# Optimization experiments

Hardware: AMD Instinct MI355X
Metric: run time of the kernel (lower is better)

Reference implementation:

```python
import jax, jax.numpy as jnp
import numpy as np

N_NODES = 50000

def setup_inputs() -> dict:
    key = jax.random.key(0)
    ks = jax.random.split(key, 4)
    x = jax.random.normal(ks[0], (N_NODES, 64), dtype=jnp.float32)
    edge_index = jax.random.randint(ks[1], (2, 800000), 0, N_NODES, dtype=jnp.int64)
    W1 = jax.random.normal(ks[2], (64, 128), dtype=jnp.float32) * (1.0 / np.sqrt(64))
    b1 = jnp.zeros((128,), dtype=jnp.float32)
    W2 = jax.random.normal(ks[3], (128, 64), dtype=jnp.float32) * (1.0 / np.sqrt(128))
    b2 = jnp.zeros((64,), dtype=jnp.float32)
    eps = jnp.zeros((1,), dtype=jnp.float32)
    return {"x": x, "edge_index": edge_index, "W1": W1, "b1": b1, "W2": W2, "b2": b2, "eps": eps}

def reference(x, edge_index, W1, b1, W2, b2, eps):
    row, col = edge_index[0], edge_index[1]
    # gather neighbor features [E, d] and scatter-add into destination nodes [N, d]
    agg = jax.ops.segment_sum(x[col], row, num_segments=x.shape[0])
    h = (1.0 + eps[0]) * x + agg
    # 2-layer MLP: Linear -> ReLU -> Linear
    h = jax.nn.relu(h @ W1 + b1)
    return h @ W2 + b2
```

## Files before the change

### kernel.cpp

```cpp
#include <hip/hip_runtime.h>

#define N_NODES 50000
#define N_EDGES 800000
#define D 64
#define H 128
#define NB512 128
#define NLIVE 98
#define CAP 8960
#define BT 2048
#define NBB 391
#define HCAP 704
#define XCB 3125
#define WPB 64

typedef __attribute__((ext_vector_type(8))) short  short8;
typedef __attribute__((ext_vector_type(4))) float  floatx4;
typedef __attribute__((ext_vector_type(4))) unsigned short ushort4v;

__device__ inline unsigned short f2bf(float f) {
    unsigned u = __builtin_bit_cast(unsigned, f);
    u += 0x7FFFu + ((u >> 16) & 1u);
    return (unsigned short)(u >> 16);
}
__device__ inline float bf2f(unsigned short b) {
    unsigned u = (unsigned)b << 16;
    return __builtin_bit_cast(float, u);
}

__global__ __launch_bounds__(256) void bin_prep(
    const int* __restrict__ row, const int* __restrict__ col,
    int* __restrict__ cursor, int* __restrict__ csr,
    const float* __restrict__ x, unsigned short* __restrict__ xb,
    const float* __restrict__ W1, unsigned short* __restrict__ w1t,
    const float* __restrict__ W2, unsigned short* __restrict__ w2t)
{
    int t = threadIdx.x;
    if (blockIdx.x >= NBB) {
        int tid = (blockIdx.x - NBB) * 256 + t;
        if (tid < 800000) {
            float4 v = ((const float4*)x)[tid];
            ushort4v o;
            o.x = f2bf(v.x); o.y = f2bf(v.y); o.z = f2bf(v.z); o.w = f2bf(v.w);
            ((ushort4v*)xb)[tid] = o;
        } else {
            int i = tid - 800000;
            if (i < D * H) {
                int k = i >> 7, n = i & 127;
                w1t[n * D + k] = f2bf(W1[i]);
            } else if (i < 2 * D * H) {
                int j = i - D * H;
                int k = j >> 6, n = j & 63;
                w2t[n * H + k] = f2bf(W2[j]);
            }
        }
        return;
    }

    __shared__ int cnt[NB512];
    __shared__ int loffs[NB512];
    __shared__ int gbase[NB512];
    __shared__ int sorted[BT];
    __shared__ int wsum[2];

    if (t < NB512) cnt[t] = 0;
    __syncthreads();

    int base = blockIdx.x * BT;
    int nloc = min(BT, N_EDGES - base);
    for (int i = t; i < nloc; i += 256)
        atomicAdd(&cnt[row[base + i] >> 9], 1);
    __syncthreads();

    int v = 0, incl = 0;
    int lane = t & 63;
    if (t < NB512) {
        v = cnt[t];
        incl = v;
        #pragma unroll
        for (int d = 1; d < 64; d <<= 1) {
            int y = __shfl_up(incl, d);
            if (lane >= d) incl += y;
        }
        if (lane == 63) wsum[t >> 6] = incl;
    }
    __syncthreads();
    if (t < NB512) {
        int add = (t >= 64) ? wsum[0] : 0;
        int excl = incl - v + add;
        loffs[t] = excl;
        if (v) gbase[t] = t * CAP + atomicAdd(&cursor[t], v);
    }
    __syncthreads();

    if (t < NB512) cnt[t] = 0;
    __syncthreads();

    for (int i = t; i < nloc; i += 256) {
        unsigned r = (unsigned)row[base + i], cc = (unsigned)col[base + i];
        int b = (int)(r >> 9);
        int lp = atomicAdd(&cnt[b], 1);
        sorted[loffs[b] + lp] = (int)((r << 16) | cc);
    }
    __syncthreads();

    for (int i = t; i < nloc; i += 256) {
        unsigned en = (unsigned)sorted[i];
        int b = (int)(en >> 25);
        int pos = gbase[b] + (i - loffs[b]);
        csr[pos] = (int)en;
    }
}

__global__ __launch_bounds__(256, 4) void gather_mlp(
    const float* __restrict__ x, const unsigned short* __restrict__ xb,
    const int* __restrict__ cursor, const int* __restrict__ csr,
    const unsigned short* __restrict__ w1t, const float* __restrict__ b1,
    const unsigned short* __restrict__ w2t, const float* __restrict__ b2,
    const float* __restrict__ eps, float* __restrict__ out)
{
    __shared__ unsigned short scol[HCAP];
    __shared__ int cnt32[32], offs[33], curs[32];
    __shared__ unsigned short HB[32][72];
    __shared__ unsigned short HID[2][16][136];

    int t = threadIdx.x, lane = t & 63, wid = t >> 6;
    int bucket = blockIdx.x >> 4;
    int sub    = blockIdx.x & 15;

    if (t < 32) cnt32[t] = 0;
    __syncthreads();

    int cntE = min(cursor[bucket], CAP);
    const int* src = csr + bucket * CAP;

    for (int i = t; i < cntE; i += 256) {
        unsigned en = (unsigned)src[i];
        int local = (int)((en >> 16) & 511u);
        if ((local >> 5) == sub) atomicAdd(&cnt32[local & 31], 1);
    }
    __syncthreads();

    if (t < 32) {
        int v = cnt32[t];
        int incl = v;
        #pragma unroll
        for (int d = 1; d < 32; d <<= 1) {
            int y = __shfl_up(incl, d);
            if (lane >= d) incl += y;
        }
        offs[t] = incl - v;
        curs[t] = incl - v;
        if (t == 31) offs[32] = incl;
    }
    __syncthreads();

    for (int i = t; i < cntE; i += 256) {
        unsigned en = (unsigned)src[i];
        int local = (int)((en >> 16) & 511u);
        if ((local >> 5) == sub) {
            int p = atomicAdd(&curs[local & 31], 1);
            if (p < HCAP) scol[p] = (unsigned short)(en & 0xFFFFu);
        }
    }
    __syncthreads();

    float ep = 1.0f + eps[0];
    int half = lane >> 5, fl = lane & 31;
    #pragma unroll 1
    for (int n2 = 0; n2 < 8; ++n2) {
        int nl = wid * 8 + n2;
        int node = bucket * 512 + sub * 32 + nl;
        int jb = min(offs[nl], HCAP), je = min(offs[nl + 1], HCAP);
        float s0a = 0.f, s1a = 0.f, s0b = 0.f, s1b = 0.f;
        float s0c = 0.f, s1c = 0.f, s0d = 0.f, s1d = 0.f;
        int j = jb;
        for (; j + 8 <= je; j += 8) {
            int c0 = scol[j + half];
            int c1 = scol[j + 2 + half];
            int c2 = scol[j + 4 + half];
            int c3 = scol[j + 6 + half];
            ushort2 p0 = *(const ushort2*)&xb[c0 * D + 2 * fl];
            ushort2 p1 = *(const ushort2*)&xb[c1 * D + 2 * fl];
            ushort2 p2 = *(const ushort2*)&xb[c2 * D + 2 * fl];
            ushort2 p3 = *(const ushort2*)&xb[c3 * D + 2 * fl];
            s0a += bf2f(p0.x); s1a += bf2f(p0.y);
            s0b += bf2f(p1.x); s1b += bf2f(p1.y);
            s0c += bf2f(p2.x); s1c += bf2f(p2.y);
            s0d += bf2f(p3.x); s1d += bf2f(p3.y);
        }
        for (; j < je; j += 2) {
            if (j + half < je) {
                int c = scol[j + half];
                ushort2 p = *(const ushort2*)&xb[c * D + 2 * fl];
                s0a += bf2f(p.x); s1a += bf2f(p.y);
            }
        }
        float s0 = (s0a + s0b) + (s0c + s0d);
        float s1 = (s1a + s1b) + (s1c + s1d);
        s0 += __shfl_xor(s0, 32);
        s1 += __shfl_xor(s1, 32);
        if (half == 0) {
            float2 xv = {0.f, 0.f};
            if (node < N_NODES) xv = *(const float2*)&x[(size_t)node * D + 2 * fl];
            ushort2 o;
            o.x = f2bf(fmaf(ep, xv.x, s0));
            o.y = f2bf(fmaf(ep, xv.y, s1));
            *(ushort2*)&HB[nl][2 * fl] = o;
        }
    }
    __syncthreads();

    int m = lane & 15, q = lane >> 4;
    if (wid < 2) {
        short8 a0 = *(const short8*)&HB[wid * 16 + m][q * 8];
        short8 a1 = *(const short8*)&HB[wid * 16 + m][32 + q * 8];

        #pragma unroll
        for (int nt = 0; nt < 8; ++nt) {
            float bias = b1[nt * 16 + m];
            floatx4 acc = {bias, bias, bias, bias};
            short8 w0 = *(const short8*)&w1t[(nt * 16 + m) * D + q * 8];
            short8 w1 = *(const short8*)&w1t[(nt * 16 + m) * D + 32 + q * 8];
            acc = __builtin_amdgcn_mfma_f32_16x16x32_bf16(a0, w0, acc, 0, 0, 0);
            acc = __builtin_amdgcn_mfma_f32_16x16x32_bf16(a1, w1, acc, 0, 0, 0);
            #pragma unroll
            for (int r = 0; r < 4; ++r) {
                float hv = fmaxf(acc[r], 0.0f);
                HID[wid][q * 4 + r][nt * 16 + m] = f2bf(hv);
            }
        }
    }
    __syncthreads();

    if (wid < 2) {
        short8 ha[4];
        #pragma unroll
        for (int kc = 0; kc < 4; ++kc)
            ha[kc] = *(const short8*)&HID[wid][m][kc * 32 + q * 8];

        #pragma unroll
        for (int nt2 = 0; nt2 < 4; ++nt2) {
            float bias = b2[nt2 * 16 + m];
            floatx4 acc = {bias, bias, bias, bias};
            #pragma unroll
            for (int kc = 0; kc < 4; ++kc) {
                short8 w = *(const short8*)&w2t[(nt2 * 16 + m) * H + kc * 32 + q * 8];
                acc = __builtin_amdgcn_mfma_f32_16x16x32_bf16(ha[kc], w, acc, 0, 0, 0);
            }
            #pragma unroll
            for (int r = 0; r < 4; ++r) {
                int n2 = bucket * 512 + sub * 32 + wid * 16 + q * 4 + r;
                if (n2 < N_NODES) out[(size_t)n2 * D + nt2 * 16 + m] = acc[r];
            }
        }
    }
}

extern "C" void kernel_launch(void* const* d_in, const int* in_sizes, int n_in,
                              void* d_out, int out_size, void* d_ws, size_t ws_size,
                              hipStream_t stream) {
    const float* x   = (const float*)d_in[0];
    const int*   ei  = (const int*)  d_in[1];
    const float* W1  = (const float*)d_in[2];
    const float* b1  = (const float*)d_in[3];
    const float* W2  = (const float*)d_in[4];
    const float* b2  = (const float*)d_in[5];
    const float* eps = (const float*)d_in[6];
    float* out = (float*)d_out;

    unsigned short* xb  = (unsigned short*)d_ws;
    unsigned short* w1t = xb + (size_t)N_NODES * D;
    unsigned short* w2t = w1t + D * H;
    int* csr    = (int*)(w2t + D * H);
    int* cursor = csr + (size_t)NB512 * CAP;

    const int* row = ei;
    const int* col = ei + N_EDGES;

    hipMemsetAsync(cursor, 0, (size_t)NB512 * sizeof(int), stream);
    bin_prep<<<NBB + XCB + WPB, 256, 0, stream>>>(row, col, cursor, csr,
                                                  x, xb, W1, w1t, W2, w2t);
    gather_mlp<<<NLIVE * 16, 256, 0, stream>>>(x, xb, cursor, csr,
                                               w1t, b1, w2t, b2, eps, out);
}
```

Measured before the change: 140.9 us.

## Split gather blocks to 16 nodes, stage matching edges once via ballot compaction

```diff
diff --git a/kernel.cpp b/kernel.cpp
--- a/kernel.cpp
+++ b/kernel.cpp
@@ -6,10 +6,10 @@
 #define H 128
 #define NB512 128
 #define NLIVE 98
-#define CAP 8960
+#define CAP 9216
 #define BT 2048
 #define NBB 391
-#define HCAP 704
+#define SCAP 448
 #define XCB 3125
 #define WPB 64
 
@@ -66,9 +66,18 @@
     __syncthreads();
 
     int base = blockIdx.x * BT;
-    int nloc = min(BT, N_EDGES - base);
-    for (int i = t; i < nloc; i += 256)
-        atomicAdd(&cnt[row[base + i] >> 9], 1);
+    #pragma unroll
+    for (int i0 = 0; i0 < BT; i0 += 1024) {
+        int ia = base + i0 + t, ib = ia + 256, ic = ia + 512, id = ia + 768;
+        int ra = row[min(ia, N_EDGES - 1)];
+        int rb = row[min(ib, N_EDGES - 1)];
+        int rc = row[min(ic, N_EDGES - 1)];
+        int rd = row[min(id, N_EDGES - 1)];
+        if (ia < N_EDGES) atomicAdd(&cnt[ra >> 9], 1);
+        if (ib < N_EDGES) atomicAdd(&cnt[rb >> 9], 1);
+        if (ic < N_EDGES) atomicAdd(&cnt[rc >> 9], 1);
+        if (id < N_EDGES) atomicAdd(&cnt[rd >> 9], 1);
+    }
     __syncthreads();
 
     int v = 0, incl = 0;
@@ -86,8 +95,7 @@
     __syncthreads();
     if (t < NB512) {
         int add = (t >= 64) ? wsum[0] : 0;
-        int excl = incl - v + add;
-        loffs[t] = excl;
+        loffs[t] = incl - v + add;
         if (v) gbase[t] = t * CAP + atomicAdd(&cursor[t], v);
     }
     __syncthreads();
@@ -95,14 +103,27 @@
     if (t < NB512) cnt[t] = 0;
     __syncthreads();
 
-    for (int i = t; i < nloc; i += 256) {
-        unsigned r = (unsigned)row[base + i], cc = (unsigned)col[base + i];
-        int b = (int)(r >> 9);
-        int lp = atomicAdd(&cnt[b], 1);
-        sorted[loffs[b] + lp] = (int)((r << 16) | cc);
-    }
-    __syncthreads();
-
+    #pragma unroll
+    for (int i0 = 0; i0 < BT; i0 += 1024) {
+        int ia = base + i0 + t, ib = ia + 256, ic = ia + 512, id = ia + 768;
+        int ca0 = min(ia, N_EDGES - 1), cb0 = min(ib, N_EDGES - 1);
+        int cc0 = min(ic, N_EDGES - 1), cd0 = min(id, N_EDGES - 1);
+        unsigned ra = (unsigned)row[ca0], rb = (unsigned)row[cb0];
+        unsigned rc = (unsigned)row[cc0], rd = (unsigned)row[cd0];
+        unsigned ka = (unsigned)col[ca0], kb = (unsigned)col[cb0];
+        unsigned kc = (unsigned)col[cc0], kd = (unsigned)col[cd0];
+        if (ia < N_EDGES) { int b = (int)(ra >> 9); int lp = atomicAdd(&cnt[b], 1);
+                            sorted[loffs[b] + lp] = (int)((ra << 16) | ka); }
+        if (ib < N_EDGES) { int b = (int)(rb >> 9); int lp = atomicAdd(&cnt[b], 1);
+                            sorted[loffs[b] + lp] = (int)((rb << 16) | kb); }
+        if (ic < N_EDGES) { int b = (int)(rc >> 9); int lp = atomicAdd(&cnt[b], 1);
+                            sorted[loffs[b] + lp] = (int)((rc << 16) | kc); }
+        if (id < N_EDGES) { int b = (int)(rd >> 9); int lp = atomicAdd(&cnt[b], 1);
+                            sorted[loffs[b] + lp] = (int)((rd << 16) | kd); }
+    }
+    __syncthreads();
+
+    int nloc = min(BT, N_EDGES - base);
     for (int i = t; i < nloc; i += 256) {
         unsigned en = (unsigned)sorted[i];
         int b = (int)(en >> 25);
@@ -111,66 +132,94 @@
     }
 }
 
-__global__ __launch_bounds__(256, 4) void gather_mlp(
+__global__ __launch_bounds__(256, 8) void gather_mlp(
     const float* __restrict__ x, const unsigned short* __restrict__ xb,
     const int* __restrict__ cursor, const int* __restrict__ csr,
     const unsigned short* __restrict__ w1t, const float* __restrict__ b1,
     const unsigned short* __restrict__ w2t, const float* __restrict__ b2,
     const float* __restrict__ eps, float* __restrict__ out)
 {
-    __shared__ unsigned short scol[HCAP];
-    __shared__ int cnt32[32], offs[33], curs[32];
-    __shared__ unsigned short HB[32][72];
-    __shared__ unsigned short HID[2][16][136];
+    __shared__ int stage[SCAP];
+    __shared__ unsigned short scol[SCAP];
+    __shared__ int cnt16[16], offs[17], curs[16], nstage;
+    __shared__ unsigned short HB[16][72];
+    __shared__ unsigned short HID[16][136];
 
     int t = threadIdx.x, lane = t & 63, wid = t >> 6;
-    int bucket = blockIdx.x >> 4;
-    int sub    = blockIdx.x & 15;
-
-    if (t < 32) cnt32[t] = 0;
+    int bucket = blockIdx.x >> 5;
+    int sub    = blockIdx.x & 31;
+
+    if (t < 16) cnt16[t] = 0;
+    if (t == 0) nstage = 0;
     __syncthreads();
 
     int cntE = min(cursor[bucket], CAP);
     const int* src = csr + bucket * CAP;
 
-    for (int i = t; i < cntE; i += 256) {
-        unsigned en = (unsigned)src[i];
-        int local = (int)((en >> 16) & 511u);
-        if ((local >> 5) == sub) atomicAdd(&cnt32[local & 31], 1);
-    }
-    __syncthreads();
-
-    if (t < 32) {
-        int v = cnt32[t];
+    #pragma unroll
+    for (int b0 = 0; b0 < CAP; b0 += 1024) {
+        int i0 = b0 + t;
+        int e0 = src[i0];
+        int e1 = src[i0 + 256];
+        int e2 = src[i0 + 512];
+        int e3 = src[i0 + 768];
+        #pragma unroll
+        for (int u = 0; u < 4; ++u) {
+            int e  = (u == 0) ? e0 : (u == 1) ? e1 : (u == 2) ? e2 : e3;
+            int ii = i0 + u * 256;
+            bool mt = (ii < cntE) &&
+                      ((((unsigned)e >> 16) & 511u) >> 4) == (unsigned)sub;
+            unsigned long long mk = __ballot(mt);
+            if (mk) {
+                int ldr = __ffsll((long long)mk) - 1;
+                int pb = 0;
+                if (lane == ldr) pb = atomicAdd(&nstage, __popcll(mk));
+                pb = __shfl(pb, ldr);
+                if (mt) {
+                    int pre = __popcll(mk & ((1ull << lane) - 1ull));
+                    int p = pb + pre;
+                    if (p < SCAP) stage[p] = e;
+                }
+            }
+        }
+    }
+    __syncthreads();
+
+    int nst = min(nstage, SCAP);
+
+    for (int i = t; i < nst; i += 256)
+        atomicAdd(&cnt16[((unsigned)stage[i] >> 16) & 15u], 1);
+    __syncthreads();
+
+    if (t < 16) {
+        int v = cnt16[t];
         int incl = v;
         #pragma unroll
-        for (int d = 1; d < 32; d <<= 1) {
+        for (int d = 1; d < 16; d <<= 1) {
             int y = __shfl_up(incl, d);
             if (lane >= d) incl += y;
         }
         offs[t] = incl - v;
         curs[t] = incl - v;
-        if (t == 31) offs[32] = incl;
-    }
-    __syncthreads();
-
-    for (int i = t; i < cntE; i += 256) {
-        unsigned en = (unsigned)src[i];
-        int local = (int)((en >> 16) & 511u);
-        if ((local >> 5) == sub) {
-            int p = atomicAdd(&curs[local & 31], 1);
-            if (p < HCAP) scol[p] = (unsigned short)(en & 0xFFFFu);
-        }
+        if (t == 15) offs[16] = incl;
+    }
+    __syncthreads();
+
+    for (int i = t; i < nst; i += 256) {
+        int en = stage[i];
+        int nl = (int)(((unsigned)en >> 16) & 15u);
+        int p = atomicAdd(&curs[nl], 1);
+        scol[p] = (unsigned short)(en & 0xFFFF);
     }
     __syncthreads();
 
     float ep = 1.0f + eps[0];
     int half = lane >> 5, fl = lane & 31;
     #pragma unroll 1
-    for (int n2 = 0; n2 < 8; ++n2) {
-        int nl = wid * 8 + n2;
-        int node = bucket * 512 + sub * 32 + nl;
-        int jb = min(offs[nl], HCAP), je = min(offs[nl + 1], HCAP);
+    for (int n2 = 0; n2 < 4; ++n2) {
+        int nl = wid * 4 + n2;
+        int node = bucket * 512 + sub * 16 + nl;
+        int jb = offs[nl], je = offs[nl + 1];
         float s0a = 0.f, s1a = 0.f, s0b = 0.f, s1b = 0.f;
         float s0c = 0.f, s1c = 0.f, s0d = 0.f, s1d = 0.f;
         int j = jb;
@@ -210,10 +259,10 @@
     }
     __syncthreads();
 
-    int m = lane & 15, q = lane >> 4;
-    if (wid < 2) {
-        short8 a0 = *(const short8*)&HB[wid * 16 + m][q * 8];
-        short8 a1 = *(const short8*)&HB[wid * 16 + m][32 + q * 8];
+    if (wid == 0) {
+        int m = lane & 15, q = lane >> 4;
+        short8 a0 = *(const short8*)&HB[m][q * 8];
+        short8 a1 = *(const short8*)&HB[m][32 + q * 8];
 
         #pragma unroll
         for (int nt = 0; nt < 8; ++nt) {
@@ -226,31 +275,28 @@
             #pragma unroll
             for (int r = 0; r < 4; ++r) {
                 float hv = fmaxf(acc[r], 0.0f);
-                HID[wid][q * 4 + r][nt * 16 + m] = f2bf(hv);
-            }
-        }
-    }
-    __syncthreads();
-
-    if (wid < 2) {
+                HID[q * 4 + r][nt * 16 + m] = f2bf(hv);
+            }
+        }
+
         short8 ha[4];
         #pragma unroll
-        for (int kc = 0; kc < 4; ++kc)
-            ha[kc] = *(const short8*)&HID[wid][m][kc * 32 + q * 8];
+        for (int kc2 = 0; kc2 < 4; ++kc2)
+            ha[kc2] = *(const short8*)&HID[m][kc2 * 32 + q * 8];
 
         #pragma unroll
         for (int nt2 = 0; nt2 < 4; ++nt2) {
             float bias = b2[nt2 * 16 + m];
             floatx4 acc = {bias, bias, bias, bias};
             #pragma unroll
-            for (int kc = 0; kc < 4; ++kc) {
-                short8 w = *(const short8*)&w2t[(nt2 * 16 + m) * H + kc * 32 + q * 8];
-                acc = __builtin_amdgcn_mfma_f32_16x16x32_bf16(ha[kc], w, acc, 0, 0, 0);
+            for (int kc2 = 0; kc2 < 4; ++kc2) {
+                short8 w = *(const short8*)&w2t[(nt2 * 16 + m) * H + kc2 * 32 + q * 8];
+                acc = __builtin_amdgcn_mfma_f32_16x16x32_bf16(ha[kc2], w, acc, 0, 0, 0);
             }
             #pragma unroll
             for (int r = 0; r < 4; ++r) {
-                int n2 = bucket * 512 + sub * 32 + wid * 16 + q * 4 + r;
-                if (n2 < N_NODES) out[(size_t)n2 * D + nt2 * 16 + m] = acc[r];
+                int nn = bucket * 512 + sub * 16 + q * 4 + r;
+                if (nn < N_NODES) out[(size_t)nn * D + nt2 * 16 + m] = acc[r];
             }
         }
     }
@@ -280,6 +326,6 @@
     hipMemsetAsync(cursor, 0, (size_t)NB512 * sizeof(int), stream);
     bin_prep<<<NBB + XCB + WPB, 256, 0, stream>>>(row, col, cursor, csr,
                                                   x, xb, W1, w1t, W2, w2t);
-    gather_mlp<<<NLIVE * 16, 256, 0, stream>>>(x, xb, cursor, csr,
+    gather_mlp<<<NLIVE * 32, 256, 0, stream>>>(x, xb, cursor, csr,
                                                w1t, b1, w2t, b2, eps, out);
 }
```

New measurement: 136.8 us. 1.03x faster.

## Add second-level subsort pass and shrink gather_mlp blocks to 16 nodes

Applied to the files above, without the earlier changes.

```diff
diff --git a/kernel.cpp b/kernel.cpp
--- a/kernel.cpp
+++ b/kernel.cpp
@@ -6,12 +6,13 @@
 #define H 128
 #define NB512 128
 #define NLIVE 98
-#define CAP 8960
+#define CAP 9216
 #define BT 2048
 #define NBB 391
-#define HCAP 704
-#define XCB 3125
-#define WPB 64
+#define TILE2 2304
+#define NSUB 32
+#define SCAP2 352
+#define CVB 798
 
 typedef __attribute__((ext_vector_type(8))) short  short8;
 typedef __attribute__((ext_vector_type(4))) float  floatx4;
@@ -27,7 +28,7 @@
     return __builtin_bit_cast(float, u);
 }
 
-__global__ __launch_bounds__(256) void bin_prep(
+__global__ __launch_bounds__(1024) void bin_prep(
     const int* __restrict__ row, const int* __restrict__ col,
     int* __restrict__ cursor, int* __restrict__ csr,
     const float* __restrict__ x, unsigned short* __restrict__ xb,
@@ -36,7 +37,7 @@
 {
     int t = threadIdx.x;
     if (blockIdx.x >= NBB) {
-        int tid = (blockIdx.x - NBB) * 256 + t;
+        int tid = (blockIdx.x - NBB) * 1024 + t;
         if (tid < 800000) {
             float4 v = ((const float4*)x)[tid];
             ushort4v o;
@@ -62,17 +63,21 @@
     __shared__ int sorted[BT];
     __shared__ int wsum[2];
 
+    int lane = t & 63;
     if (t < NB512) cnt[t] = 0;
     __syncthreads();
 
     int base = blockIdx.x * BT;
-    int nloc = min(BT, N_EDGES - base);
-    for (int i = t; i < nloc; i += 256)
-        atomicAdd(&cnt[row[base + i] >> 9], 1);
+    int ia = base + t, ib = ia + 1024;
+    int ca = min(ia, N_EDGES - 1), cb = min(ib, N_EDGES - 1);
+    unsigned ra = (unsigned)row[ca], rb = (unsigned)row[cb];
+    unsigned ka = (unsigned)col[ca], kb = (unsigned)col[cb];
+    bool va = ia < N_EDGES, vb = ib < N_EDGES;
+    if (va) atomicAdd(&cnt[ra >> 9], 1);
+    if (vb) atomicAdd(&cnt[rb >> 9], 1);
     __syncthreads();
 
     int v = 0, incl = 0;
-    int lane = t & 63;
     if (t < NB512) {
         v = cnt[t];
         incl = v;
@@ -86,8 +91,7 @@
     __syncthreads();
     if (t < NB512) {
         int add = (t >= 64) ? wsum[0] : 0;
-        int excl = incl - v + add;
-        loffs[t] = excl;
+        loffs[t] = incl - v + add;
         if (v) gbase[t] = t * CAP + atomicAdd(&cursor[t], v);
     }
     __syncthreads();
@@ -95,15 +99,14 @@
     if (t < NB512) cnt[t] = 0;
     __syncthreads();
 
-    for (int i = t; i < nloc; i += 256) {
-        unsigned r = (unsigned)row[base + i], cc = (unsigned)col[base + i];
-        int b = (int)(r >> 9);
-        int lp = atomicAdd(&cnt[b], 1);
-        sorted[loffs[b] + lp] = (int)((r << 16) | cc);
-    }
-    __syncthreads();
-
-    for (int i = t; i < nloc; i += 256) {
+    if (va) { int b = (int)(ra >> 9); int lp = atomicAdd(&cnt[b], 1);
+              sorted[loffs[b] + lp] = (int)((ra << 16) | ka); }
+    if (vb) { int b = (int)(rb >> 9); int lp = atomicAdd(&cnt[b], 1);
+              sorted[loffs[b] + lp] = (int)((rb << 16) | kb); }
+    __syncthreads();
+
+    int nloc = min(BT, N_EDGES - base);
+    for (int i = t; i < nloc; i += 1024) {
         unsigned en = (unsigned)sorted[i];
         int b = (int)(en >> 25);
         int pos = gbase[b] + (i - loffs[b]);
@@ -111,66 +114,120 @@
     }
 }
 
-__global__ __launch_bounds__(256, 4) void gather_mlp(
+__global__ __launch_bounds__(256) void subsort(
+    const int* __restrict__ cursor, const int* __restrict__ csr,
+    int* __restrict__ cursor2, int* __restrict__ csr2)
+{
+    __shared__ int sorted[TILE2];
+    __shared__ int cnt32[32], loffs[32], gbase[32], curs[32];
+
+    int t = threadIdx.x, lane = t & 63;
+    int bucket = blockIdx.x >> 2;
+    int tile   = blockIdx.x & 3;
+
+    int cntE = min(cursor[bucket], CAP);
+    int tbeg = tile * TILE2;
+    int nloc = max(min(tbeg + TILE2, cntE) - tbeg, 0);
+    const int* src = csr + bucket * CAP + tbeg;
+
+    if (t < 32) cnt32[t] = 0;
+    __syncthreads();
+
+    for (int i = t; i < nloc; i += 256)
+        atomicAdd(&cnt32[(((unsigned)src[i] >> 16) & 511u) >> 4], 1);
+    __syncthreads();
+
+    if (t < 32) {
+        int v = cnt32[t];
+        int incl = v;
+        #pragma unroll
+        for (int d = 1; d < 32; d <<= 1) {
+            int y = __shfl_up(incl, d);
+            if (lane >= d) incl += y;
+        }
+        loffs[t] = incl - v;
+        curs[t]  = incl - v;
+        gbase[t] = v ? atomicAdd(&cursor2[bucket * 32 + t], v) : 0;
+    }
+    __syncthreads();
+
+    for (int i = t; i < nloc; i += 256) {
+        unsigned e = (unsigned)src[i];
+        int local = (int)((e >> 16) & 511u);
+        int p = atomicAdd(&curs[local >> 4], 1);
+        sorted[p] = (int)(((unsigned)local << 16) | (e & 0xFFFFu));
+    }
+    __syncthreads();
+
+    for (int i = t; i < nloc; i += 256) {
+        unsigned en = (unsigned)sorted[i];
+        int sub = (int)(en >> 20);
+        int rel = gbase[sub] + (i - loffs[sub]);
+        if (rel < SCAP2)
+            csr2[(bucket * 32 + sub) * SCAP2 + rel] =
+                (int)(((en >> 16) & 15u) << 16 | (en & 0xFFFFu));
+    }
+}
+
+__global__ __launch_bounds__(256, 8) void gather_mlp(
     const float* __restrict__ x, const unsigned short* __restrict__ xb,
-    const int* __restrict__ cursor, const int* __restrict__ csr,
+    const int* __restrict__ cursor2, const int* __restrict__ csr2,
     const unsigned short* __restrict__ w1t, const float* __restrict__ b1,
     const unsigned short* __restrict__ w2t, const float* __restrict__ b2,
     const float* __restrict__ eps, float* __restrict__ out)
 {
-    __shared__ unsigned short scol[HCAP];
-    __shared__ int cnt32[32], offs[33], curs[32];
-    __shared__ unsigned short HB[32][72];
-    __shared__ unsigned short HID[2][16][136];
+    __shared__ int ent[SCAP2];
+    __shared__ unsigned short scol[SCAP2];
+    __shared__ int cnt16[16], offs[17], curs[16];
+    __shared__ unsigned short HB[16][72];
+    __shared__ unsigned short HID[16][136];
 
     int t = threadIdx.x, lane = t & 63, wid = t >> 6;
-    int bucket = blockIdx.x >> 4;
-    int sub    = blockIdx.x & 15;
-
-    if (t < 32) cnt32[t] = 0;
-    __syncthreads();
-
-    int cntE = min(cursor[bucket], CAP);
-    const int* src = csr + bucket * CAP;
-
-    for (int i = t; i < cntE; i += 256) {
-        unsigned en = (unsigned)src[i];
-        int local = (int)((en >> 16) & 511u);
-        if ((local >> 5) == sub) atomicAdd(&cnt32[local & 31], 1);
-    }
-    __syncthreads();
-
-    if (t < 32) {
-        int v = cnt32[t];
+    int bs = blockIdx.x;
+    int bucket = bs >> 5, sub = bs & 31;
+
+    if (t < 16) cnt16[t] = 0;
+    __syncthreads();
+
+    int n2 = min(cursor2[bs], SCAP2);
+    const int* src = csr2 + (size_t)bs * SCAP2;
+
+    for (int i = t; i < n2; i += 256) {
+        int e = src[i];
+        ent[i] = e;
+        atomicAdd(&cnt16[((unsigned)e >> 16) & 15u], 1);
+    }
+    __syncthreads();
+
+    if (t < 16) {
+        int v = cnt16[t];
         int incl = v;
         #pragma unroll
-        for (int d = 1; d < 32; d <<= 1) {
+        for (int d = 1; d < 16; d <<= 1) {
             int y = __shfl_up(incl, d);
             if (lane >= d) incl += y;
         }
         offs[t] = incl - v;
         curs[t] = incl - v;
-        if (t == 31) offs[32] = incl;
-    }
-    __syncthreads();
-
-    for (int i = t; i < cntE; i += 256) {
-        unsigned en = (unsigned)src[i];
-        int local = (int)((en >> 16) & 511u);
-        if ((local >> 5) == sub) {
-            int p = atomicAdd(&curs[local & 31], 1);
-            if (p < HCAP) scol[p] = (unsigned short)(en & 0xFFFFu);
-        }
+        if (t == 15) offs[16] = incl;
+    }
+    __syncthreads();
+
+    for (int i = t; i < n2; i += 256) {
+        int e = ent[i];
+        int nl = (int)(((unsigned)e >> 16) & 15u);
+        int p = atomicAdd(&curs[nl], 1);
+        scol[p] = (unsigned short)(e & 0xFFFF);
     }
     __syncthreads();
 
     float ep = 1.0f + eps[0];
     int half = lane >> 5, fl = lane & 31;
     #pragma unroll 1
-    for (int n2 = 0; n2 < 8; ++n2) {
-        int nl = wid * 8 + n2;
-        int node = bucket * 512 + sub * 32 + nl;
-        int jb = min(offs[nl], HCAP), je = min(offs[nl + 1], HCAP);
+    for (int nn = 0; nn < 4; ++nn) {
+        int nl = wid * 4 + nn;
+        int node = bucket * 512 + sub * 16 + nl;
+        int jb = offs[nl], je = offs[nl + 1];
         float s0a = 0.f, s1a = 0.f, s0b = 0.f, s1b = 0.f;
         float s0c = 0.f, s1c = 0.f, s0d = 0.f, s1d = 0.f;
         int j = jb;
@@ -210,10 +267,10 @@
     }
     __syncthreads();
 
-    int m = lane & 15, q = lane >> 4;
-    if (wid < 2) {
-        short8 a0 = *(const short8*)&HB[wid * 16 + m][q * 8];
-        short8 a1 = *(const short8*)&HB[wid * 16 + m][32 + q * 8];
+    if (wid == 0) {
+        int m = lane & 15, q = lane >> 4;
+        short8 a0 = *(const short8*)&HB[m][q * 8];
+        short8 a1 = *(const short8*)&HB[m][32 + q * 8];
 
         #pragma unroll
         for (int nt = 0; nt < 8; ++nt) {
@@ -226,31 +283,28 @@
             #pragma unroll
             for (int r = 0; r < 4; ++r) {
                 float hv = fmaxf(acc[r], 0.0f);
-                HID[wid][q * 4 + r][nt * 16 + m] = f2bf(hv);
-            }
-        }
-    }
-    __syncthreads();
-
-    if (wid < 2) {
+                HID[q * 4 + r][nt * 16 + m] = f2bf(hv);
+            }
+        }
+
         short8 ha[4];
         #pragma unroll
-        for (int kc = 0; kc < 4; ++kc)
-            ha[kc] = *(const short8*)&HID[wid][m][kc * 32 + q * 8];
+        for (int kc2 = 0; kc2 < 4; ++kc2)
+            ha[kc2] = *(const short8*)&HID[m][kc2 * 32 + q * 8];
 
         #pragma unroll
         for (int nt2 = 0; nt2 < 4; ++nt2) {
             float bias = b2[nt2 * 16 + m];
             floatx4 acc = {bias, bias, bias, bias};
             #pragma unroll
-            for (int kc = 0; kc < 4; ++kc) {
-                short8 w = *(const short8*)&w2t[(nt2 * 16 + m) * H + kc * 32 + q * 8];
-                acc = __builtin_amdgcn_mfma_f32_16x16x32_bf16(ha[kc], w, acc, 0, 0, 0);
+            for (int kc2 = 0; kc2 < 4; ++kc2) {
+                short8 w = *(const short8*)&w2t[(nt2 * 16 + m) * H + kc2 * 32 + q * 8];
+                acc = __builtin_amdgcn_mfma_f32_16x16x32_bf16(ha[kc2], w, acc, 0, 0, 0);
             }
             #pragma unroll
             for (int r = 0; r < 4; ++r) {
-                int n2 = bucket * 512 + sub * 32 + wid * 16 + q * 4 + r;
-                if (n2 < N_NODES) out[(size_t)n2 * D + nt2 * 16 + m] = acc[r];
+                int nn2 = bucket * 512 + sub * 16 + q * 4 + r;
+                if (nn2 < N_NODES) out[(size_t)nn2 * D + nt2 * 16 + m] = acc[r];
             }
         }
     }
@@ -271,15 +325,18 @@
     unsigned short* xb  = (unsigned short*)d_ws;
     unsigned short* w1t = xb + (size_t)N_NODES * D;
     unsigned short* w2t = w1t + D * H;
-    int* csr    = (int*)(w2t + D * H);
-    int* cursor = csr + (size_t)NB512 * CAP;
+    int* csr     = (int*)(w2t + D * H);
+    int* csr2    = csr + (size_t)NB512 * CAP;
+    int* cursor  = csr2 + (size_t)NLIVE * 32 * SCAP2;
+    int* cursor2 = cursor + NB512;
 
     const int* row = ei;
     const int* col = ei + N_EDGES;
 
-    hipMemsetAsync(cursor, 0, (size_t)NB512 * sizeof(int), stream);
-    bin_prep<<<NBB + XCB + WPB, 256, 0, stream>>>(row, col, cursor, csr,
-                                                  x, xb, W1, w1t, W2, w2t);
-    gather_mlp<<<NLIVE * 16, 256, 0, stream>>>(x, xb, cursor, csr,
+    hipMemsetAsync(cursor, 0, (size_t)(NB512 + NLIVE * 32) * sizeof(int), stream);
+    bin_prep<<<NBB + CVB, 1024, 0, stream>>>(row, col, cursor, csr,
+                                             x, xb, W1, w1t, W2, w2t);
+    subsort<<<NLIVE * 4, 256, 0, stream>>>(cursor, csr, cursor2, csr2);
+    gather_mlp<<<NLIVE * 32, 256, 0, stream>>>(x, xb, cursor2, csr2,
                                                w1t, b1, w2t, b2, eps, out);
 }
```

After: 128.0 us. 1.1x faster.
